# Kernel tuning notes

Measured on AMD Instinct MI355X. Metric: run time of the kernel, lower is better.

## Reference

```python
import jax, jax.numpy as jnp
import numpy as np

N_NODES = 100000
N_EDGES = 1600000
D_IN = 128
D_OUT = 128


def setup_inputs() -> dict:
    key = jax.random.key(0)
    k1, k2, k3, k4, k5, k6 = jax.random.split(key, 6)
    x = jax.random.normal(k1, (N_NODES, D_IN), dtype=jnp.float32)
    edge_index = jax.random.randint(k2, (2, N_EDGES), 0, N_NODES, dtype=jnp.int64)
    edge_weight = jax.random.uniform(k3, (N_EDGES,), dtype=jnp.float32)
    # Linear(in_features=128, out_features=128, bias=True) parameters
    bound = 1.0 / np.sqrt(D_IN)
    W = jax.random.uniform(k4, (D_OUT, D_IN), minval=-bound, maxval=bound, dtype=jnp.float32)
    b = jax.random.uniform(k5, (D_OUT,), minval=-bound, maxval=bound, dtype=jnp.float32)
    return {
        "x": x,
        "edge_index": edge_index,
        "edge_weight": edge_weight,
        "W": W,
        "b": b,
        "vertex_cnt": N_NODES,
        "rule_cnt": 0,
    }


def reference(x, edge_index, edge_weight, W, b, vertex_cnt, rule_cnt):
    # KPropagate: edge-based message passing.
    # messages[e] = edge_weight[e] * x[src[e]]; out[dst] = sum of messages into dst.
    src = edge_index[0]
    dst = edge_index[1]
    msgs = x[src] * edge_weight[:, None]          # [E, D_IN]
    agg = jax.ops.segment_sum(msgs, dst, num_segments=vertex_cnt)  # [N, D_IN]
    # Dense linear projection: y = agg @ W^T + b
    return agg @ W.T + b
```

## Files before the change

kernel.cpp:

```cpp
#include <hip/hip_runtime.h>
#include <hip/hip_bf16.h>

#define D 128
#define RT 64
#define BK 64
#define CAP 2048
#define SUBCAP 256
#define PAD 16

typedef __attribute__((ext_vector_type(8))) short short8;
typedef __attribute__((ext_vector_type(4))) float floatx4;

__device__ __forceinline__ ushort f2bf(float v) {
  return __hip_bfloat16_raw(__float2bfloat16(v)).x;
}
__device__ __forceinline__ float bf2f(ushort u) {
  return __uint_as_float((unsigned)u << 16);
}

__device__ __forceinline__ int xcd_id() {
  int v;
  asm volatile("s_getreg_b32 %0, hwreg(HW_REG_XCC_ID)" : "=s"(v));
  return v & 7;
}

__global__ __launch_bounds__(256) void k1_gemm_fill(
    const float* __restrict__ x, const float* __restrict__ W,
    ushort* __restrict__ y, const int* __restrict__ ei,
    const float* __restrict__ ew, int* __restrict__ cursor,
    int2* __restrict__ bucket, int N, int E, int GB) {
  if (blockIdx.x >= GB) {
    int sb = xcd_id();
    int e = (blockIdx.x - GB) * 256 + threadIdx.x;
    if (e < E) {
      int s = ei[e];
      int d = ei[E + e];
      float w = ew[e];
      int bk = d >> 6;
      int p = atomicAdd(&cursor[(bk * 8 + sb) * PAD], 1);
      if (p < SUBCAP)
        bucket[(long long)bk * CAP + sb * SUBCAP + p] =
            make_int2(s | ((d & 63) << 26), __float_as_int(w));
    }
    return;
  }
  __shared__ __align__(16) ushort sX[RT * 136];
  __shared__ __align__(16) ushort sW[128 * 136];

  int tid = threadIdx.x;
  int rowBase = blockIdx.x * RT;

#pragma unroll
  for (int it = 0; it < 16; it++) {
    int i = tid + it * 256;
    int r = i >> 5;
    int c4 = i & 31;
    float4 v = *(const float4*)(W + r * 128 + c4 * 4);
    *(ushort4*)&sW[r * 136 + c4 * 4] =
        make_ushort4(f2bf(v.x), f2bf(v.y), f2bf(v.z), f2bf(v.w));
  }
#pragma unroll
  for (int it = 0; it < 8; it++) {
    int i = tid + it * 256;
    int r = i >> 5;
    int c4 = i & 31;
    int row = rowBase + r;
    float4 v = (row < N) ? *(const float4*)(x + (long long)row * 128 + c4 * 4)
                         : make_float4(0.f, 0.f, 0.f, 0.f);
    *(ushort4*)&sX[r * 136 + c4 * 4] =
        make_ushort4(f2bf(v.x), f2bf(v.y), f2bf(v.z), f2bf(v.w));
  }
  __syncthreads();

  int wv = tid >> 6;
  int lane = tid & 63;
  int m = lane & 15;
  int q = lane >> 4;

  const ushort* aRow = &sX[(wv * 16 + m) * 136 + q * 8];
  const ushort* bRow = &sW[m * 136 + q * 8];

  floatx4 acc[8];
#pragma unroll
  for (int ct = 0; ct < 8; ct++) acc[ct] = (floatx4){0.f, 0.f, 0.f, 0.f};

#pragma unroll
  for (int ks = 0; ks < 4; ks++) {
    short8 a = *(const short8*)(aRow + ks * 32);
#pragma unroll
    for (int ct = 0; ct < 8; ct++) {
      short8 b = *(const short8*)(bRow + ct * 16 * 136 + ks * 32);
      acc[ct] = __builtin_amdgcn_mfma_f32_16x16x32_bf16(a, b, acc[ct], 0, 0, 0);
    }
  }

  int row0 = rowBase + wv * 16 + q * 4;
#pragma unroll
  for (int r = 0; r < 4; r++) {
    int row = row0 + r;
    if (row < N) {
      ushort* yp = y + (long long)row * 128 + m;
#pragma unroll
      for (int ct = 0; ct < 8; ct++) yp[ct * 16] = f2bf(acc[ct][r]);
    }
  }
}

__global__ __launch_bounds__(256) void sort_gather(
    const ushort* __restrict__ y, const int2* __restrict__ bucket,
    const int* __restrict__ cursor, const float* __restrict__ bias,
    float* __restrict__ out, int N) {
  __shared__ __align__(16) int2 smd[CAP];
  __shared__ int sdeg[BK];
  __shared__ int soffs[BK];
  __shared__ int scur[BK];

  int tid = threadIdx.x;
  int bk = blockIdx.x;
  long long base = (long long)bk * CAP;

  if (tid < BK) sdeg[tid] = 0;
  __syncthreads();
#pragma unroll
  for (int sb = 0; sb < 8; sb++) {
    int c = min(cursor[(bk * 8 + sb) * PAD], SUBCAP);
    for (int i = tid; i < c; i += 256) {
      unsigned v = (unsigned)bucket[base + sb * SUBCAP + i].x;
      atomicAdd(&sdeg[v >> 26], 1);
    }
  }
  __syncthreads();
  if (tid < BK) {
    int s = 0;
    for (int j = 0; j < tid; j++) s += sdeg[j];
    soffs[tid] = s;
    scur[tid] = s;
  }
  __syncthreads();
#pragma unroll
  for (int sb = 0; sb < 8; sb++) {
    int c = min(cursor[(bk * 8 + sb) * PAD], SUBCAP);
    for (int i = tid; i < c; i += 256) {
      int2 md = bucket[base + sb * SUBCAP + i];
      int d = (unsigned)md.x >> 26;
      int pos = atomicAdd(&scur[d], 1);
      smd[pos] = md;
    }
  }
  __syncthreads();

  int wv = tid >> 6;
  int lane = tid & 63;
  const ushort2* yv = (const ushort2*)y;
  float2 bb = ((const float2*)bias)[lane];

  for (int nd = wv; nd < BK; nd += 4) {
    int node = bk * BK + nd;
    if (node >= N) continue;
    int st = soffs[nd];
    int c = sdeg[nd];
    float ax = 0.f, ay = 0.f;
    int j = 0;
    for (; j + 4 <= c; j += 4) {
      int2 m0 = smd[st + j];
      int2 m1 = smd[st + j + 1];
      int2 m2 = smd[st + j + 2];
      int2 m3 = smd[st + j + 3];
      int s0 = m0.x & 0x03FFFFFF, s1 = m1.x & 0x03FFFFFF;
      int s2 = m2.x & 0x03FFFFFF, s3 = m3.x & 0x03FFFFFF;
      float w0 = __int_as_float(m0.y), w1 = __int_as_float(m1.y);
      float w2 = __int_as_float(m2.y), w3 = __int_as_float(m3.y);
      ushort2 u0 = yv[(long long)s0 * 64 + lane];
      ushort2 u1 = yv[(long long)s1 * 64 + lane];
      ushort2 u2 = yv[(long long)s2 * 64 + lane];
      ushort2 u3 = yv[(long long)s3 * 64 + lane];
      ax += w0 * bf2f(u0.x) + w1 * bf2f(u1.x) + w2 * bf2f(u2.x) +
            w3 * bf2f(u3.x);
      ay += w0 * bf2f(u0.y) + w1 * bf2f(u1.y) + w2 * bf2f(u2.y) +
            w3 * bf2f(u3.y);
    }
    for (; j < c; j++) {
      int2 m0 = smd[st + j];
      int s0 = m0.x & 0x03FFFFFF;
      float w0 = __int_as_float(m0.y);
      ushort2 u0 = yv[(long long)s0 * 64 + lane];
      ax += w0 * bf2f(u0.x);
      ay += w0 * bf2f(u0.y);
    }
    float2 o = {ax + bb.x, ay + bb.y};
    ((float2*)out)[(long long)node * 64 + lane] = o;
  }
}

extern "C" void kernel_launch(void* const* d_in, const int* in_sizes, int n_in,
                              void* d_out, int out_size, void* d_ws,
                              size_t ws_size, hipStream_t stream) {
  const float* x = (const float*)d_in[0];
  const int* ei = (const int*)d_in[1];
  const float* ew = (const float*)d_in[2];
  const float* W = (const float*)d_in[3];
  const float* b = (const float*)d_in[4];

  int N = in_sizes[0] / D;
  int E = in_sizes[2];
  int NBK = (N + BK - 1) / BK;

  int* cursor = (int*)d_ws;
  int2* bucket = (int2*)(cursor + (size_t)NBK * 8 * PAD);
  ushort* y = (ushort*)(bucket + (size_t)NBK * CAP);

  hipMemsetAsync(cursor, 0, (size_t)NBK * 8 * PAD * sizeof(int), stream);

  int GB = (N + RT - 1) / RT;
  int FB = (E + 255) / 256;
  k1_gemm_fill<<<GB + FB, 256, 0, stream>>>(x, W, y, ei, ew, cursor, bucket, N,
                                            E, GB);
  sort_gather<<<NBK, 256, 0, stream>>>(y, bucket, cursor, b, (float*)d_out, N);
}
```

Before: 250.3 us.

## Prepack W into MFMA fragment layout and read fragments from global memory

A small kernel now converts W to bf16 once per call and stores it in the exact per-lane MFMA B-fragment order. The GEMM blocks then read these fragments straight from global/L2 instead of staging all of W into LDS. This removes per-block W conversion and LDS traffic and reduces LDS use, which may raise occupancy. Input streams (x, edge index, weights) are also read with nontemporal loads to limit cache pollution. The cost is an extra kernel launch, and the B operands now come from global memory with higher latency.

```diff
diff --git a/kernel.cpp b/kernel.cpp
--- a/kernel.cpp
+++ b/kernel.cpp
@@ -24,8 +24,25 @@
   return v & 7;
 }
 
+__global__ __launch_bounds__(256) void prep_w(const float* __restrict__ W,
+                                              ushort* __restrict__ Wp) {
+  int g = blockIdx.x * 256 + threadIdx.x;
+  int ct = g >> 8;
+  int ks = (g >> 6) & 3;
+  int lane = g & 63;
+  int m = lane & 15;
+  int q = lane >> 4;
+  const float* p = W + (ct * 16 + m) * 128 + ks * 32 + q * 8;
+  float4 v0 = *(const float4*)p;
+  float4 v1 = *(const float4*)(p + 4);
+  *(ushort4*)(Wp + (long long)g * 8) =
+      make_ushort4(f2bf(v0.x), f2bf(v0.y), f2bf(v0.z), f2bf(v0.w));
+  *(ushort4*)(Wp + (long long)g * 8 + 4) =
+      make_ushort4(f2bf(v1.x), f2bf(v1.y), f2bf(v1.z), f2bf(v1.w));
+}
+
 __global__ __launch_bounds__(256) void k1_gemm_fill(
-    const float* __restrict__ x, const float* __restrict__ W,
+    const float* __restrict__ x, const ushort* __restrict__ Wp,
     ushort* __restrict__ y, const int* __restrict__ ei,
     const float* __restrict__ ew, int* __restrict__ cursor,
     int2* __restrict__ bucket, int N, int E, int GB) {
@@ -33,9 +50,9 @@
     int sb = xcd_id();
     int e = (blockIdx.x - GB) * 256 + threadIdx.x;
     if (e < E) {
-      int s = ei[e];
-      int d = ei[E + e];
-      float w = ew[e];
+      int s = __builtin_nontemporal_load(ei + e);
+      int d = __builtin_nontemporal_load(ei + E + e);
+      float w = __builtin_nontemporal_load(ew + e);
       int bk = d >> 6;
       int p = atomicAdd(&cursor[(bk * 8 + sb) * PAD], 1);
       if (p < SUBCAP)
@@ -45,28 +62,22 @@
     return;
   }
   __shared__ __align__(16) ushort sX[RT * 136];
-  __shared__ __align__(16) ushort sW[128 * 136];
 
   int tid = threadIdx.x;
   int rowBase = blockIdx.x * RT;
 
-#pragma unroll
-  for (int it = 0; it < 16; it++) {
-    int i = tid + it * 256;
-    int r = i >> 5;
-    int c4 = i & 31;
-    float4 v = *(const float4*)(W + r * 128 + c4 * 4);
-    *(ushort4*)&sW[r * 136 + c4 * 4] =
-        make_ushort4(f2bf(v.x), f2bf(v.y), f2bf(v.z), f2bf(v.w));
-  }
 #pragma unroll
   for (int it = 0; it < 8; it++) {
     int i = tid + it * 256;
     int r = i >> 5;
     int c4 = i & 31;
     int row = rowBase + r;
-    float4 v = (row < N) ? *(const float4*)(x + (long long)row * 128 + c4 * 4)
-                         : make_float4(0.f, 0.f, 0.f, 0.f);
+    floatx4 v;
+    if (row < N)
+      v = __builtin_nontemporal_load(
+          (const floatx4*)(x + (long long)row * 128 + c4 * 4));
+    else
+      v = (floatx4){0.f, 0.f, 0.f, 0.f};
     *(ushort4*)&sX[r * 136 + c4 * 4] =
         make_ushort4(f2bf(v.x), f2bf(v.y), f2bf(v.z), f2bf(v.w));
   }
@@ -78,7 +89,7 @@
   int q = lane >> 4;
 
   const ushort* aRow = &sX[(wv * 16 + m) * 136 + q * 8];
-  const ushort* bRow = &sW[m * 136 + q * 8];
+  const ushort* wBase = Wp + (long long)lane * 8;
 
   floatx4 acc[8];
 #pragma unroll
@@ -89,7 +100,7 @@
     short8 a = *(const short8*)(aRow + ks * 32);
 #pragma unroll
     for (int ct = 0; ct < 8; ct++) {
-      short8 b = *(const short8*)(bRow + ct * 16 * 136 + ks * 32);
+      short8 b = *(const short8*)(wBase + (ct * 256 + ks * 64) * 8);
       acc[ct] = __builtin_amdgcn_mfma_f32_16x16x32_bf16(a, b, acc[ct], 0, 0, 0);
     }
   }
@@ -206,14 +217,16 @@
   int NBK = (N + BK - 1) / BK;
 
   int* cursor = (int*)d_ws;
-  int2* bucket = (int2*)(cursor + (size_t)NBK * 8 * PAD);
+  ushort* Wp = (ushort*)(cursor + (size_t)NBK * 8 * PAD);
+  int2* bucket = (int2*)(Wp + 128 * 128);
   ushort* y = (ushort*)(bucket + (size_t)NBK * CAP);
 
-  hipMemsetAsync(cursor, 0, (size_t)NBK * 8 * PAD * sizeof(int), stream);
+  (void)hipMemsetAsync(cursor, 0, (size_t)NBK * 8 * PAD * sizeof(int), stream);
+  prep_w<<<8, 256, 0, stream>>>(W, Wp);
 
   int GB = (N + RT - 1) / RT;
   int FB = (E + 255) / 256;
-  k1_gemm_fill<<<GB + FB, 256, 0, stream>>>(x, W, y, ei, ew, cursor, bucket, N,
-                                            E, GB);
+  k1_gemm_fill<<<GB + FB, 256, 0, stream>>>(x, Wp, y, ei, ew, cursor, bucket,
+                                            N, E, GB);
   sort_gather<<<NBK, 256, 0, stream>>>(y, bucket, cursor, b, (float*)d_out, N);
 }
```

Measured after the change: 251.3 us. Within noise of the previous version (+0.4%).
